# Kernel tuning notes

Measured on AMD Instinct MI355X. Metric: run time of the kernel, lower is better.

## Reference

```python
import jax, jax.numpy as jnp
import numpy as np

BS, N, K, S = 512, 500, 100, 96  # batch, nodes per sample, kriged nodes per sample, seq_len
HID, AUG = 32, 2
TAU = 0.1


def setup_inputs() -> dict:
    key = jax.random.key(0)
    ks = jax.random.split(key, 8)
    x = jax.random.normal(ks[0], (BS * N, S), jnp.float32)
    y = jax.random.normal(ks[1], (BS * N, S), jnp.float32)
    W1 = jax.random.normal(ks[2], (S, HID), jnp.float32) / np.sqrt(S)
    b1 = jnp.zeros((HID,), jnp.float32)
    W2 = jax.random.normal(ks[3], (HID, AUG), jnp.float32) / np.sqrt(HID)
    b2 = jnp.zeros((AUG,), jnp.float32)
    # unique node indices per sample (torch index-assign with dups is ill-defined)
    perm_keys = jax.random.split(ks[4], BS)
    krig_idx = jax.vmap(lambda k: jax.random.permutation(k, N)[:K])(perm_keys).astype(jnp.int32)
    idx_of_node = jnp.full((BS,), N, jnp.int32)  # nodes per sample
    mask = (jax.random.uniform(ks[5], (BS * K, S)) > 0.1).astype(jnp.float32)
    gumbel = jax.random.gumbel(ks[6], (BS * K, AUG), jnp.float32)
    return {"x": x, "y": y, "W1": W1, "b1": b1, "W2": W2, "b2": b2,
            "mask": mask, "gumbel": gumbel, "krig_idx": krig_idx,
            "idx_of_node": idx_of_node}


def reference(x, y, W1, b1, W2, b2, mask, gumbel, krig_idx, idx_of_node):
    bs, k = krig_idx.shape
    num_nodes = x.shape[0] // bs
    s = x.shape[1]
    # gather kriged node series: [bs, num_nodes, S] -> [bs*K, S]
    y3 = y.reshape(bs, num_nodes, s)
    smp = jnp.take_along_axis(y3, krig_idx[:, :, None], axis=1).reshape(bs * k, s)
    # tiny MLP on gathered features (krig_feat == smp, same gather done twice in torch)
    h = jax.nn.relu(smp @ W1 + b1)
    logits = h @ W2 + b2
    # hard gumbel-softmax, straight-through
    y_soft = jax.nn.softmax((logits + gumbel) / TAU, axis=-1)
    y_hard = jax.nn.one_hot(jnp.argmax(y_soft, axis=-1), logits.shape[-1], dtype=y_soft.dtype)
    gb = y_hard - jax.lax.stop_gradient(y_soft) + y_soft  # [bs*K, 2]
    # data_aug = [zeros, mask*smp] (detached); sum over aug dim == gb[:,1]*masked
    val = gb[:, 1:2] * jax.lax.stop_gradient(mask * smp)  # [bs*K, S]
    # flat row indices: per-sample offsets from shifted cumsum of idx_of_node
    offs = jnp.cumsum(jnp.concatenate([jnp.zeros((1,), idx_of_node.dtype), idx_of_node])[:-1])
    flat = (offs[:, None] + krig_idx).reshape(-1)  # [bs*K]
    return x.at[flat].set(val)
```

## Files before the change

kernel.cpp:

```cpp
#include <hip/hip_runtime.h>

#define BSZ 512
#define NN  500
#define KK  100
#define SS  96
#define HIDN 32
#define ROWS (BSZ * NN)
#define NF4  (ROWS * SS / 4)
#define F4PR (SS / 4)

typedef float vf4 __attribute__((ext_vector_type(4)));

__global__ __launch_bounds__(512) void prep_kernel(const int* __restrict__ idx_of_node,
                                                   int* __restrict__ offs,
                                                   int* __restrict__ flag) {
    if (blockIdx.x == 0) {
        __shared__ int buf[BSZ];
        int t = threadIdx.x;
        int v = idx_of_node[t];
        buf[t] = v;
        __syncthreads();
        int acc = v;
        for (int d = 1; d < BSZ; d <<= 1) {
            int add = (t >= d) ? buf[t - d] : 0;
            __syncthreads();
            acc += add;
            buf[t] = acc;
            __syncthreads();
        }
        offs[t] = acc - v;
    }
    int4* f4 = reinterpret_cast<int4*>(flag);
    int n4 = ROWS / 4;
    for (int i = blockIdx.x * 512 + threadIdx.x; i < n4; i += gridDim.x * 512)
        f4[i] = make_int4(-1, -1, -1, -1);
}

__global__ __launch_bounds__(256) void gate_kernel(
    const float* __restrict__ y, const float* __restrict__ W1,
    const float* __restrict__ b1, const float* __restrict__ W2,
    const float* __restrict__ b2, const float* __restrict__ gumbel,
    const int* __restrict__ krig_idx, const int* __restrict__ offs,
    int* __restrict__ flag, float* __restrict__ gate) {
    __shared__ float4 w1s[SS * HIDN / 4];
    __shared__ float b1s[HIDN];
    __shared__ float w2s[HIDN * 2];
    __shared__ float b2s[2];
    for (int i = threadIdx.x; i < SS * HIDN / 4; i += 256)
        w1s[i] = reinterpret_cast<const float4*>(W1)[i];
    if (threadIdx.x < HIDN) b1s[threadIdx.x] = b1[threadIdx.x];
    if (threadIdx.x < 2 * HIDN) w2s[threadIdx.x] = W2[threadIdx.x];
    if (threadIdx.x < 2) b2s[threadIdx.x] = b2[threadIdx.x];
    __syncthreads();

    int r = blockIdx.x * 256 + threadIdx.x;
    if (r >= BSZ * KK) return;
    int b = r / KK;
    int node = krig_idx[r];
    const float4* yrow = reinterpret_cast<const float4*>(y + (size_t)(b * NN + node) * SS);

    float h[HIDN];
#pragma unroll
    for (int j = 0; j < HIDN; ++j) h[j] = b1s[j];
#pragma unroll
    for (int s4 = 0; s4 < F4PR; ++s4) {
        float4 v = yrow[s4];
        float vv[4] = {v.x, v.y, v.z, v.w};
        const float4* wbase = &w1s[s4 * 4 * (HIDN / 4)];
#pragma unroll
        for (int q = 0; q < 4; ++q) {
#pragma unroll
            for (int j4 = 0; j4 < HIDN / 4; ++j4) {
                float4 w = wbase[q * (HIDN / 4) + j4];
                h[j4 * 4 + 0] += vv[q] * w.x;
                h[j4 * 4 + 1] += vv[q] * w.y;
                h[j4 * 4 + 2] += vv[q] * w.z;
                h[j4 * 4 + 3] += vv[q] * w.w;
            }
        }
    }
    float l0 = b2s[0], l1 = b2s[1];
#pragma unroll
    for (int j = 0; j < HIDN; ++j) {
        float hr = fmaxf(h[j], 0.0f);
        l0 += hr * w2s[j * 2 + 0];
        l1 += hr * w2s[j * 2 + 1];
    }
    float g0 = gumbel[r * 2 + 0], g1 = gumbel[r * 2 + 1];
    gate[r] = (l1 + g1 > l0 + g0) ? 1.0f : 0.0f;
    flag[offs[b] + node] = r;
}

__global__ __launch_bounds__(256) void fuse_kernel(
    const vf4* __restrict__ x4, const vf4* __restrict__ y4,
    const vf4* __restrict__ mask4, const float* __restrict__ gate,
    const int* __restrict__ flag, const int* __restrict__ krig_idx,
    vf4* __restrict__ out4) {
    int idx = blockIdx.x * 256 + threadIdx.x;
    int stride = gridDim.x * 256;
    for (; idx < NF4; idx += stride) {
        int row = idx / F4PR;
        int c = idx - row * F4PR;
        int r = flag[row];
        vf4 o;
        if (r < 0) {
            o = __builtin_nontemporal_load(x4 + idx);
        } else {
            int b = r / KK;
            int node = krig_idx[r];
            float g = gate[r];
            vf4 m = mask4[r * F4PR + c];
            vf4 v = y4[(b * NN + node) * F4PR + c];
            o = g * m * v;
        }
        __builtin_nontemporal_store(o, out4 + idx);
    }
}

extern "C" void kernel_launch(void* const* d_in, const int* in_sizes, int n_in,
                              void* d_out, int out_size, void* d_ws, size_t ws_size,
                              hipStream_t stream) {
    const float* x      = (const float*)d_in[0];
    const float* y      = (const float*)d_in[1];
    const float* W1     = (const float*)d_in[2];
    const float* b1     = (const float*)d_in[3];
    const float* W2     = (const float*)d_in[4];
    const float* b2     = (const float*)d_in[5];
    const float* mask   = (const float*)d_in[6];
    const float* gumbel = (const float*)d_in[7];
    const int* krig_idx = (const int*)d_in[8];
    const int* idx_of_node = (const int*)d_in[9];
    float* out = (float*)d_out;

    int* offs = (int*)d_ws;
    int* flag = offs + BSZ;
    float* gate = (float*)(flag + ROWS);

    prep_kernel<<<128, 512, 0, stream>>>(idx_of_node, offs, flag);

    int rows = BSZ * KK;
    gate_kernel<<<(rows + 255) / 256, 256, 0, stream>>>(
        y, W1, b1, W2, b2, gumbel, krig_idx, offs, flag, gate);

    fuse_kernel<<<8192, 256, 0, stream>>>(
        reinterpret_cast<const vf4*>(x), reinterpret_cast<const vf4*>(y),
        reinterpret_cast<const vf4*>(mask), gate, flag, krig_idx,
        reinterpret_cast<vf4*>(out));
}
```

Baseline: 66.97 us.

## Batch fuse kernel loads into register slots for memory-level parallelism

Reworks the fuse kernel so each thread issues twelve independent x and flag loads up front, then overwrites the kriged rows with the gated masked values, then stores everything. The grid shrinks to 2048 blocks so that fixed slot count covers the whole array. The goal is more outstanding memory requests per thread instead of a dependent flag-then-branch chain. In exchange it reads x even for rows that get replaced, which is extra traffic, and it uses more registers.

```diff
diff --git a/kernel.cpp b/kernel.cpp
--- a/kernel.cpp
+++ b/kernel.cpp
@@ -8,6 +8,9 @@
 #define ROWS (BSZ * NN)
 #define NF4  (ROWS * SS / 4)
 #define F4PR (SS / 4)
+#define NSLOT 12
+#define FUSE_BLOCKS 2048
+#define FUSE_STRIDE (FUSE_BLOCKS * 256)
 
 typedef float vf4 __attribute__((ext_vector_type(4)));
 
@@ -96,24 +99,39 @@
     const vf4* __restrict__ mask4, const float* __restrict__ gate,
     const int* __restrict__ flag, const int* __restrict__ krig_idx,
     vf4* __restrict__ out4) {
-    int idx = blockIdx.x * 256 + threadIdx.x;
-    int stride = gridDim.x * 256;
-    for (; idx < NF4; idx += stride) {
-        int row = idx / F4PR;
-        int c = idx - row * F4PR;
-        int r = flag[row];
-        vf4 o;
-        if (r < 0) {
-            o = __builtin_nontemporal_load(x4 + idx);
+    const int t = blockIdx.x * 256 + threadIdx.x;
+
+    vf4 xv[NSLOT];
+    int fr[NSLOT];
+#pragma unroll
+    for (int k = 0; k < NSLOT; ++k) {
+        int idx = t + k * FUSE_STRIDE;
+        if (idx < NF4) {
+            xv[k] = x4[idx];
+            fr[k] = flag[idx / F4PR];
         } else {
+            fr[k] = -1;
+        }
+    }
+#pragma unroll
+    for (int k = 0; k < NSLOT; ++k) {
+        int r = fr[k];
+        if (r >= 0) {
+            int idx = t + k * FUSE_STRIDE;
+            int row = idx / F4PR;
+            int c = idx - row * F4PR;
             int b = r / KK;
             int node = krig_idx[r];
             float g = gate[r];
             vf4 m = mask4[r * F4PR + c];
             vf4 v = y4[(b * NN + node) * F4PR + c];
-            o = g * m * v;
+            xv[k] = g * m * v;
         }
-        __builtin_nontemporal_store(o, out4 + idx);
+    }
+#pragma unroll
+    for (int k = 0; k < NSLOT; ++k) {
+        int idx = t + k * FUSE_STRIDE;
+        if (idx < NF4) __builtin_nontemporal_store(xv[k], out4 + idx);
     }
 }
 
@@ -142,7 +160,7 @@
     gate_kernel<<<(rows + 255) / 256, 256, 0, stream>>>(
         y, W1, b1, W2, b2, gumbel, krig_idx, offs, flag, gate);
 
-    fuse_kernel<<<8192, 256, 0, stream>>>(
+    fuse_kernel<<<FUSE_BLOCKS, 256, 0, stream>>>(
         reinterpret_cast<const vf4*>(x), reinterpret_cast<const vf4*>(y),
         reinterpret_cast<const vf4*>(mask), gate, flag, krig_idx,
         reinterpret_cast<vf4*>(out));
```

Result: no change. 68.30 us (+2.0%).
